# Performance work log

Measured on AMD Instinct MI355X. Metric: run time of the kernel, lower is better.

Reference implementation:

```python
import jax, jax.numpy as jnp
import numpy as np

D_MODEL = 1024
NUM_HEADS = 16
D_K = D_MODEL // NUM_HEADS
B, S = 4, 2048


def setup_inputs() -> dict:
    key = jax.random.key(0)
    ks = jax.random.split(key, 11)
    scale = 1.0 / np.sqrt(D_MODEL)
    inp = {
        "query": jax.random.normal(ks[0], (B, S, D_MODEL), dtype=jnp.float32),
        "key": jax.random.normal(ks[1], (B, S, D_MODEL), dtype=jnp.float32),
        "value": jax.random.normal(ks[2], (B, S, D_MODEL), dtype=jnp.float32),
        "mask": jnp.tril(jnp.ones((S, S), dtype=jnp.int32))[None, None, :, :],
        "Wq": jax.random.normal(ks[3], (D_MODEL, D_MODEL), dtype=jnp.float32) * scale,
        "bq": jax.random.normal(ks[4], (D_MODEL,), dtype=jnp.float32) * scale,
        "Wk": jax.random.normal(ks[5], (D_MODEL, D_MODEL), dtype=jnp.float32) * scale,
        "bk": jax.random.normal(ks[6], (D_MODEL,), dtype=jnp.float32) * scale,
        "Wv": jax.random.normal(ks[7], (D_MODEL, D_MODEL), dtype=jnp.float32) * scale,
        "bv": jax.random.normal(ks[8], (D_MODEL,), dtype=jnp.float32) * scale,
        "Wo": jax.random.normal(ks[9], (D_MODEL, D_MODEL), dtype=jnp.float32) * scale,
        "bo": jax.random.normal(ks[10], (D_MODEL,), dtype=jnp.float32) * scale,
    }
    return inp


def reference(query, key, value, mask, Wq, bq, Wk, bk, Wv, bv, Wo, bo):
    b, s, _ = query.shape
    # Linear projections (torch Linear: x @ W.T + b), split into heads -> [B,H,S,Dk]
    Q = (query @ Wq.T + bq).reshape(b, s, NUM_HEADS, D_K).transpose(0, 2, 1, 3)
    K = (key @ Wk.T + bk).reshape(b, s, NUM_HEADS, D_K).transpose(0, 2, 1, 3)
    V = (value @ Wv.T + bv).reshape(b, s, NUM_HEADS, D_K).transpose(0, 2, 1, 3)
    scores = jnp.einsum("bhqd,bhkd->bhqk", Q, K) / jnp.sqrt(jnp.float32(D_K))
    scores = jnp.where(mask == 0, -jnp.inf, scores)
    attn = jax.nn.softmax(scores, axis=-1)  # dropout p=0.0 -> identity
    x = jnp.einsum("bhqk,bhkd->bhqd", attn, V)
    x = x.transpose(0, 2, 1, 3).reshape(b, s, D_MODEL)
    return x @ Wo.T + bo
```

## Files before the change

### kernel.cpp

```cpp
#include <hip/hip_runtime.h>
#include <cstdint>

#define DM   1024
#define NH   16
#define DKd  64
#define Bb   4
#define Ss   2048

using bf16x8_t = __attribute__((ext_vector_type(8))) __bf16;
using bf16x2_t = __attribute__((ext_vector_type(2))) __bf16;
using f32x4_t  = __attribute__((ext_vector_type(4))) float;
using u16x4_t  = __attribute__((ext_vector_type(4))) unsigned short;
using u16x8_t  = __attribute__((ext_vector_type(8))) unsigned short;
using u32x2_t  = __attribute__((ext_vector_type(2))) unsigned int;

#define MFMA16(a, b, c) __builtin_amdgcn_mfma_f32_16x16x32_bf16((a), (b), (c), 0, 0, 0)

__device__ __forceinline__ void mfma_k16(f32x4_t& c, u32x2_t a, u32x2_t b) {
  asm("v_mfma_f32_16x16x16_bf16 %0, %1, %2, %0" : "+v"(c) : "v"(a), "v"(b));
}

__device__ __forceinline__ unsigned short f2bf(float f) {
  union { float f; unsigned u; } v; v.f = f;
  unsigned r = v.u + 0x7fffu + ((v.u >> 16) & 1u);
  return (unsigned short)(r >> 16);
}

__device__ __forceinline__ void gl16(const void* g, void* l) {
  __builtin_amdgcn_global_load_lds(
      (const __attribute__((address_space(1))) void*)g,
      (__attribute__((address_space(3))) void*)l, 16, 0, 0);
}

struct CvtArgs {
  const float* src[4];
  unsigned short* dst[4];
  int n[4];
};

__global__ void cvt_kernel(CvtArgs a) {
  const int seg = blockIdx.y;
  const float* __restrict__ s = a.src[seg];
  unsigned short* __restrict__ d = a.dst[seg];
  const int n = a.n[seg];
  const int step = gridDim.x * blockDim.x * 4;
  for (int i = (blockIdx.x * blockDim.x + threadIdx.x) * 4; i < n; i += step) {
    f32x4_t v = *(const f32x4_t*)(s + i);
    u16x4_t r;
    r[0] = f2bf(v[0]); r[1] = f2bf(v[1]); r[2] = f2bf(v[2]); r[3] = f2bf(v[3]);
    *(u16x4_t*)(d + i) = r;
  }
}

struct GemmArgs {
  const unsigned short* A[3];
  const float* A32[3];
  const unsigned short* W[3];
  const float* bias[3];
  void* out[3];
  float scl[3];
  int epi[3];
};

__device__ __forceinline__ void gemm_epilogue(
    const GemmArgs& ga, int z, int epi, float scl, const float* bias,
    f32x4_t (&acc)[4][4], int m0, int n0, int wm, int wn, int qr, int kg) {
#pragma unroll
  for (int ni = 0; ni < 4; ++ni) {
    const int col = n0 + wn * 64 + ni * 16 + qr;
    const float bi = bias[col];
#pragma unroll
    for (int mi = 0; mi < 4; ++mi) {
      const int mb = m0 + wm * 64 + mi * 16 + kg * 4;
      float vv[4];
#pragma unroll
      for (int j = 0; j < 4; ++j) vv[j] = (acc[mi][ni][j] + bi) * scl;
      if (epi == 0) {
        unsigned short* O = (unsigned short*)ga.out[z];
#pragma unroll
        for (int j = 0; j < 4; ++j) {
          const int m = mb + j;
          O[(size_t)((m >> 11) * NH + (col >> 6)) * (Ss * DKd) +
            (size_t)(m & (Ss - 1)) * DKd + (col & 63)] = f2bf(vv[j]);
        }
      } else if (epi == 2) {
        unsigned short* O = (unsigned short*)ga.out[z];
        u16x4_t r;
#pragma unroll
        for (int j = 0; j < 4; ++j) r[j] = f2bf(vv[j]);
        const int b = mb >> 11, s = mb & (Ss - 1);
        *(u16x4_t*)&O[((size_t)(b * NH + (col >> 6)) * DKd + (col & 63)) * Ss + s] = r;
      } else {
        float* O = (float*)ga.out[z];
#pragma unroll
        for (int j = 0; j < 4; ++j) O[(size_t)(mb + j) * 1024 + col] = vv[j];
      }
    }
  }
}

__global__ __launch_bounds__(256, 3) void gemm_qkv(GemmArgs ga) {
  const int L = blockIdx.x + 8 * (blockIdx.y + 64 * blockIdx.z);
  const int xcd = L & 7;
  const int sidx = L >> 3;
  const int xw = sidx & 7;
  const int grp = sidx >> 3;
  const int z = grp >> 3;
  const int yw = (grp & 7) * 8 + xcd;

  const float* __restrict__ A32 = ga.A32[z];
  const unsigned short* __restrict__ W = ga.W[z];
  const float* __restrict__ bias = ga.bias[z];
  const float scl = ga.scl[z];
  const int epi = ga.epi[z];

  __shared__ __align__(16) unsigned short sA[128 * 32];
  __shared__ __align__(16) unsigned short sB[2][128 * 32];

  const int tid  = threadIdx.x;
  const int lane = tid & 63;
  const int wid  = tid >> 6;
  const int wm   = wid >> 1, wn = wid & 1;
  const int m0 = yw * 128, n0 = xw * 128;
  const int qr = lane & 15, kg = lane >> 4;

  const int e0 = tid * 8;
  const int e1 = e0 + 2048;
  const int r0 = e0 >> 5, c0 = e0 & 31;
  const int r1 = e1 >> 5, c1 = e1 & 31;

  f32x4_t acc[4][4];
#pragma unroll
  for (int mi = 0; mi < 4; ++mi)
#pragma unroll
    for (int ni = 0; ni < 4; ++ni) acc[mi][ni] = {0.f, 0.f, 0.f, 0.f};

  const float* Ar0 = A32 + (size_t)(m0 + r0) * 1024 + c0;
  const float* Ar1 = A32 + (size_t)(m0 + r1) * 1024 + c1;

  f32x4_t areg[2][4];

#define LDA(par, kn)                                        \
  do {                                                      \
    areg[par][0] = *(const f32x4_t*)(Ar0 + (kn) * 32 + 0);  \
    areg[par][1] = *(const f32x4_t*)(Ar0 + (kn) * 32 + 4);  \
    areg[par][2] = *(const f32x4_t*)(Ar1 + (kn) * 32 + 0);  \
    areg[par][3] = *(const f32x4_t*)(Ar1 + (kn) * 32 + 4);  \
  } while (0)

#define WRA(par)                                            \
  do {                                                      \
    u16x8_t w0_, w1_;                                       \
    _Pragma("unroll") for (int j = 0; j < 4; ++j) {         \
      w0_[j] = f2bf(areg[par][0][j]);                       \
      w0_[4 + j] = f2bf(areg[par][1][j]);                   \
      w1_[j] = f2bf(areg[par][2][j]);                       \
      w1_[4 + j] = f2bf(areg[par][3][j]);                   \
    }                                                       \
    *(u16x8_t*)&sA[e0] = w0_;                               \
    *(u16x8_t*)&sA[e1] = w1_;                               \
  } while (0)

#define LDW(buf, kn)                                                      \
  do {                                                                    \
    gl16(W + (size_t)(n0 + r0) * 1024 + (kn) * 32 + c0, &sB[buf][e0]);    \
    gl16(W + (size_t)(n0 + r1) * 1024 + (kn) * 32 + c1, &sB[buf][e1]);    \
  } while (0)

  LDA(0, 0);
  LDW(0, 0);
  asm volatile("s_waitcnt vmcnt(2)" ::: "memory");
  WRA(0);
  LDA(1, 1);
  LDW(1, 1);
  asm volatile("s_waitcnt vmcnt(6)" ::: "memory");
  asm volatile("s_waitcnt lgkmcnt(0)" ::: "memory");
  __builtin_amdgcn_s_barrier();

#pragma unroll
  for (int kt = 0; kt < 32; ++kt) {
    bf16x8_t af[4], bfr[4];
#pragma unroll
    for (int i = 0; i < 4; ++i) {
      af[i]  = *(const bf16x8_t*)&sA[(wm * 64 + i * 16 + qr) * 32 + kg * 8];
      bfr[i] = *(const bf16x8_t*)&sB[kt & 1][(wn * 64 + i * 16 + qr) * 32 + kg * 8];
    }
    __builtin_amdgcn_s_setprio(1);
#pragma unroll
    for (int mi = 0; mi < 4; ++mi)
#pragma unroll
      for (int ni = 0; ni < 4; ++ni)
        acc[mi][ni] = MFMA16(af[mi], bfr[ni], acc[mi][ni]);
    __builtin_amdgcn_s_setprio(0);
    __builtin_amdgcn_s_barrier();

    if (kt < 31) {
      asm volatile("s_waitcnt vmcnt(2)" ::: "memory");
      WRA((kt + 1) & 1);
      if (kt + 2 < 32) {
        LDA(kt & 1, kt + 2);
        LDW(kt & 1, kt + 2);
        asm volatile("s_waitcnt vmcnt(6)" ::: "memory");
      } else {
        asm volatile("s_waitcnt vmcnt(0)" ::: "memory");
      }
      asm volatile("s_waitcnt lgkmcnt(0)" ::: "memory");
      __builtin_amdgcn_s_barrier();
    }
  }
#undef LDA
#undef WRA
#undef LDW

  gemm_epilogue(ga, z, epi, scl, bias, acc, m0, n0, wm, wn, qr, kg);
}

__global__ __launch_bounds__(256, 4) void gemm_bt(GemmArgs ga) {
  const int L = blockIdx.x + 8 * (blockIdx.y + 64 * blockIdx.z);
  const int xcd = L & 7;
  const int sidx = L >> 3;
  const int xw = sidx & 7;
  const int grp = sidx >> 3;
  const int z = grp >> 3;
  const int yw = (grp & 7) * 8 + xcd;

  const unsigned short* __restrict__ A = ga.A[z];
  const unsigned short* __restrict__ W = ga.W[z];
  const float* __restrict__ bias = ga.bias[z];
  const float scl = ga.scl[z];
  const int epi = ga.epi[z];

  __shared__ __align__(16) unsigned short sA[128 * 32];
  __shared__ __align__(16) unsigned short sB[128 * 32];

  const int tid  = threadIdx.x;
  const int lane = tid & 63;
  const int wid  = tid >> 6;
  const int wm   = wid >> 1, wn = wid & 1;
  const int m0 = yw * 128, n0 = xw * 128;
  const int qr = lane & 15, kg = lane >> 4;

  const int e0 = tid * 8;
  const int e1 = e0 + 2048;
  const int r0 = e0 >> 5, c0 = e0 & 31;
  const int r1 = e1 >> 5, c1 = e1 & 31;

  f32x4_t acc[4][4];
#pragma unroll
  for (int mi = 0; mi < 4; ++mi)
#pragma unroll
    for (int ni = 0; ni < 4; ++ni) acc[mi][ni] = {0.f, 0.f, 0.f, 0.f};

  for (int kt = 0; kt < 32; ++kt) {
    const int k0 = kt * 32;
    gl16(A + (size_t)(m0 + r0) * 1024 + k0 + c0, &sA[e0]);
    gl16(A + (size_t)(m0 + r1) * 1024 + k0 + c1, &sA[e1]);
    gl16(W + (size_t)(n0 + r0) * 1024 + k0 + c0, &sB[e0]);
    gl16(W + (size_t)(n0 + r1) * 1024 + k0 + c1, &sB[e1]);
    __syncthreads();

    bf16x8_t af[4], bfr[4];
#pragma unroll
    for (int i = 0; i < 4; ++i) {
      af[i]  = *(const bf16x8_t*)&sA[(wm * 64 + i * 16 + qr) * 32 + kg * 8];
      bfr[i] = *(const bf16x8_t*)&sB[(wn * 64 + i * 16 + qr) * 32 + kg * 8];
    }
#pragma unroll
    for (int mi = 0; mi < 4; ++mi)
#pragma unroll
      for (int ni = 0; ni < 4; ++ni)
        acc[mi][ni] = MFMA16(af[mi], bfr[ni], acc[mi][ni]);
    __syncthreads();
  }

  gemm_epilogue(ga, z, epi, scl, bias, acc, m0, n0, wm, wn, qr, kg);
}

__global__ __launch_bounds__(256, 3) void attn_kernel(
    const unsigned short* __restrict__ Qp, const unsigned short* __restrict__ Kp,
    const unsigned short* __restrict__ Vt, unsigned short* __restrict__ X) {
  const int x = blockIdx.x, y = blockIdx.y;
  const int bh = x * 8 + (y & 7);
  const int pr = y >> 3;

  const int tid = threadIdx.x, lane = tid & 63, w = tid >> 6;
  const int qr = lane & 15, kg = lane >> 4;

  const unsigned short* Qb = Qp + (size_t)bh * Ss * DKd;
  const unsigned short* Kb = Kp + (size_t)bh * Ss * DKd;
  const unsigned short* Vb = Vt + (size_t)bh * Ss * DKd;

  __shared__ __align__(16) unsigned short kbuf[2][4096];
  __shared__ __align__(16) unsigned short vbuf[2][4096];

  const int R0 = tid >> 3, c80 = (tid & 7) ^ (R0 & 7);
  const int R1 = R0 + 32,  c81 = (tid & 7) ^ (R1 & 7);

  const int bq = bh >> 4, hh = bh & 15;

#pragma unroll
  for (int half = 0; half < 2; ++half) {
    const int jsub = half == 0 ? (15 - pr) : pr;
    const int qbase = jsub * 128;
    const int ntile = 2 * jsub + 2;
    const int qrowA = qbase + w * 32 + qr;
    const int qrowB = qrowA + 16;

    const bf16x8_t qfA0 = *(const bf16x8_t*)&Qb[(size_t)qrowA * DKd + kg * 8];
    const bf16x8_t qfA1 = *(const bf16x8_t*)&Qb[(size_t)qrowA * DKd + 32 + kg * 8];
    const bf16x8_t qfB0 = *(const bf16x8_t*)&Qb[(size_t)qrowB * DKd + kg * 8];
    const bf16x8_t qfB1 = *(const bf16x8_t*)&Qb[(size_t)qrowB * DKd + 32 + kg * 8];

    float lA = 0.f, lB = 0.f;
    f32x4_t o[2][4];
#pragma unroll
    for (int g = 0; g < 2; ++g)
#pragma unroll
      for (int nd = 0; nd < 4; ++nd) o[g][nd] = {0.f, 0.f, 0.f, 0.f};

    int cur = 0;
    gl16(Kb + (size_t)R0 * DKd + c80 * 8, &kbuf[0][tid * 8]);
    gl16(Kb + (size_t)R1 * DKd + c81 * 8, &kbuf[0][tid * 8 + 2048]);
    gl16(Vb + (size_t)R0 * Ss + c80 * 8, &vbuf[0][tid * 8]);
    gl16(Vb + (size_t)R1 * Ss + c81 * 8, &vbuf[0][tid * 8 + 2048]);
    __syncthreads();

    for (int t = 0; t < ntile; ++t) {
      if (t + 1 < ntile) {
        const int kv0 = (t + 1) * 64;
        const int nb = cur ^ 1;
        gl16(Kb + (size_t)(kv0 + R0) * DKd + c80 * 8, &kbuf[nb][tid * 8]);
        gl16(Kb + (size_t)(kv0 + R1) * DKd + c81 * 8, &kbuf[nb][tid * 8 + 2048]);
        gl16(Vb + (size_t)R0 * Ss + kv0 + c80 * 8, &vbuf[nb][tid * 8]);
        gl16(Vb + (size_t)R1 * Ss + kv0 + c81 * 8, &vbuf[nb][tid * 8 + 2048]);
      }

      const bool act = !(w < 2 && t == 2 * jsub + 1);
      if (act) {
        f32x4_t sA_[4], sB_[4];
#pragma unroll
        for (int ni = 0; ni < 4; ++ni) {
          sA_[ni] = {-8.f, -8.f, -8.f, -8.f};
          sB_[ni] = {-8.f, -8.f, -8.f, -8.f};
        }
        __builtin_amdgcn_s_setprio(1);
#pragma unroll
        for (int ni = 0; ni < 4; ++ni) {
          const int R = ni * 16 + qr;
          const bf16x8_t kf0 =
              *(const bf16x8_t*)&kbuf[cur][(R * 8 + (kg ^ (qr & 7))) * 8];
          const bf16x8_t kf1 =
              *(const bf16x8_t*)&kbuf[cur][(R * 8 + ((4 + kg) ^ (qr & 7))) * 8];
          sA_[ni] = MFMA16(kf0, qfA0, sA_[ni]);
          sA_[ni] = MFMA16(kf1, qfA1, sA_[ni]);
          sB_[ni] = MFMA16(kf0, qfB0, sB_[ni]);
          sB_[ni] = MFMA16(kf1, qfB1, sB_[ni]);
        }
        __builtin_amdgcn_s_setprio(0);

        if (t >= 2 * jsub) {
          const int off = (t == 2 * jsub) ? 0 : 64;
          const int rA = w * 32 + qr - off;
#pragma unroll
          for (int ni = 0; ni < 4; ++ni)
#pragma unroll
            for (int j = 0; j < 4; ++j) {
              const int c = ni * 16 + kg * 4 + j;
              if (c > rA) sA_[ni][j] = -1.0e30f;
              if (c > rA + 16) sB_[ni][j] = -1.0e30f;
            }
        }

        u32x2_t pbA[4], pbB[4];
#pragma unroll
        for (int ni = 0; ni < 4; ++ni) {
          float pa0 = exp2f(sA_[ni][0]), pa1 = exp2f(sA_[ni][1]);
          float pa2 = exp2f(sA_[ni][2]), pa3 = exp2f(sA_[ni][3]);
          lA += (pa0 + pa1) + (pa2 + pa3);
          bf16x2_t lo, hi;
          lo[0] = (__bf16)pa0; lo[1] = (__bf16)pa1;
          hi[0] = (__bf16)pa2; hi[1] = (__bf16)pa3;
          pbA[ni][0] = __builtin_bit_cast(unsigned, lo);
          pbA[ni][1] = __builtin_bit_cast(unsigned, hi);
          float pb0 = exp2f(sB_[ni][0]), pb1 = exp2f(sB_[ni][1]);
          float pb2 = exp2f(sB_[ni][2]), pb3 = exp2f(sB_[ni][3]);
          lB += (pb0 + pb1) + (pb2 + pb3);
          bf16x2_t lo2, hi2;
          lo2[0] = (__bf16)pb0; lo2[1] = (__bf16)pb1;
          hi2[0] = (__bf16)pb2; hi2[1] = (__bf16)pb3;
          pbB[ni][0] = __builtin_bit_cast(unsigned, lo2);
          pbB[ni][1] = __builtin_bit_cast(unsigned, hi2);
        }
        asm volatile("s_nop 1");

        __builtin_amdgcn_s_setprio(1);
#pragma unroll
        for (int nd = 0; nd < 4; ++nd) {
          const int rb = (qr + 16 * nd) * 64 + 4 * (kg & 1);
          const int ch = kg >> 1, sw = qr & 7;
          u32x2_t va0 = *(const u32x2_t*)&vbuf[cur][rb + 8 * ((ch + 0) ^ sw)];
          u32x2_t va1 = *(const u32x2_t*)&vbuf[cur][rb + 8 * ((ch + 2) ^ sw)];
          u32x2_t va2 = *(const u32x2_t*)&vbuf[cur][rb + 8 * ((ch + 4) ^ sw)];
          u32x2_t va3 = *(const u32x2_t*)&vbuf[cur][rb + 8 * ((ch + 6) ^ sw)];
          mfma_k16(o[0][nd], va0, pbA[0]);
          mfma_k16(o[0][nd], va1, pbA[1]);
          mfma_k16(o[0][nd], va2, pbA[2]);
          mfma_k16(o[0][nd], va3, pbA[3]);
          mfma_k16(o[1][nd], va0, pbB[0]);
          mfma_k16(o[1][nd], va1, pbB[1]);
          mfma_k16(o[1][nd], va2, pbB[2]);
          mfma_k16(o[1][nd], va3, pbB[3]);
        }
        __builtin_amdgcn_s_setprio(0);
      }

      __syncthreads();
      cur ^= 1;
    }

    float lsA = lA, lsB = lB;
    lsA += __shfl_xor(lsA, 16); lsA += __shfl_xor(lsA, 32);
    lsB += __shfl_xor(lsB, 16); lsB += __shfl_xor(lsB, 32);
    const float invA = 1.0f / lsA, invB = 1.0f / lsB;
#pragma unroll
    for (int nd = 0; nd < 4; ++nd) {
      u16x4_t rA, rB;
#pragma unroll
      for (int j = 0; j < 4; ++j) {
        rA[j] = f2bf(o[0][nd][j] * invA);
        rB[j] = f2bf(o[1][nd][j] * invB);
      }
      const int d = nd * 16 + kg * 4;
      *(u16x4_t*)&X[(size_t)(bq * Ss + qrowA) * DM + hh * DKd + d] = rA;
      *(u16x4_t*)&X[(size_t)(bq * Ss + qrowB) * DM + hh * DKd + d] = rB;
    }
  }
}

extern "C" void kernel_launch(void* const* d_in, const int* in_sizes, int n_in,
                              void* d_out, int out_size, void* d_ws, size_t ws_size,
                              hipStream_t stream) {
  const float* q  = (const float*)d_in[0];
  const float* k  = (const float*)d_in[1];
  const float* v  = (const float*)d_in[2];
  const float* Wq = (const float*)d_in[4];
  const float* bq = (const float*)d_in[5];
  const float* Wk = (const float*)d_in[6];
  const float* bk = (const float*)d_in[7];
  const float* Wv = (const float*)d_in[8];
  const float* bv = (const float*)d_in[9];
  const float* Wo = (const float*)d_in[10];
  const float* bo = (const float*)d_in[11];

  const size_t NIN = (size_t)Bb * Ss * DM;
  const size_t NW  = (size_t)DM * DM;

  unsigned short* ws  = (unsigned short*)d_ws;
  unsigned short* Wqb = ws;
  unsigned short* Wkb = Wqb + NW;
  unsigned short* Wvb = Wkb + NW;
  unsigned short* Wob = Wvb + NW;
  unsigned short* qb  = Wob + NW;
  unsigned short* Qp  = qb + NIN;
  unsigned short* Kp  = Qp + NIN;
  unsigned short* Vt  = Kp + NIN;
  unsigned short* X   = qb;

  CvtArgs ca{};
  ca.src[0] = Wq; ca.dst[0] = Wqb; ca.n[0] = (int)NW;
  ca.src[1] = Wk; ca.dst[1] = Wkb; ca.n[1] = (int)NW;
  ca.src[2] = Wv; ca.dst[2] = Wvb; ca.n[2] = (int)NW;
  ca.src[3] = Wo; ca.dst[3] = Wob; ca.n[3] = (int)NW;
  cvt_kernel<<<dim3(256, 4), 256, 0, stream>>>(ca);

  const float SC = 0.18033688011112042f;

  GemmArgs g1{};
  g1.A32[0] = q;   g1.A32[1] = k;   g1.A32[2] = v;
  g1.W[0] = Wqb;   g1.W[1] = Wkb;   g1.W[2] = Wvb;
  g1.bias[0] = bq; g1.bias[1] = bk; g1.bias[2] = bv;
  g1.out[0] = Qp;  g1.out[1] = Kp;  g1.out[2] = Vt;
  g1.scl[0] = SC;  g1.scl[1] = 1.f; g1.scl[2] = 1.f;
  g1.epi[0] = 0;   g1.epi[1] = 0;   g1.epi[2] = 2;
  gemm_qkv<<<dim3(8, 64, 3), 256, 0, stream>>>(g1);

  attn_kernel<<<dim3(8, 64), 256, 0, stream>>>(Qp, Kp, Vt, X);

  GemmArgs g2{};
  g2.A[0] = X; g2.W[0] = Wob; g2.bias[0] = bo; g2.out[0] = d_out;
  g2.scl[0] = 1.f; g2.epi[0] = 1;
  gemm_bt<<<dim3(8, 64, 1), 256, 0, stream>>>(g2);
}
```

Measured before the change: 179.2 us.

## Load fp32 A tiles directly to LDS and convert to bf16 at fragment read

The QKV projection GEMM now streams fp32 activation tiles straight into shared memory with direct global-to-LDS loads in an XOR-swizzled layout. It converts them to bf16 per fragment when reading, instead of staging through registers and writing bf16 into LDS. The double-buffered, register-prefetched software pipeline is replaced by a single-buffer load/sync/compute/sync loop, and occupancy is raised to 4 blocks. This frees registers and the conversion stores, but loses the overlap of loads with MFMA. It also repeats the fp32-to-bf16 conversion across the two waves that share each A row.

```diff
diff --git a/kernel.cpp b/kernel.cpp
--- a/kernel.cpp
+++ b/kernel.cpp
@@ -99,7 +99,7 @@
   }
 }
 
-__global__ __launch_bounds__(256, 3) void gemm_qkv(GemmArgs ga) {
+__global__ __launch_bounds__(256, 4) void gemm_qkv(GemmArgs ga) {
   const int L = blockIdx.x + 8 * (blockIdx.y + 64 * blockIdx.z);
   const int xcd = L & 7;
   const int sidx = L >> 3;
@@ -114,8 +114,8 @@
   const float scl = ga.scl[z];
   const int epi = ga.epi[z];
 
-  __shared__ __align__(16) unsigned short sA[128 * 32];
-  __shared__ __align__(16) unsigned short sB[2][128 * 32];
+  __shared__ __align__(16) float sA32[128 * 32];
+  __shared__ __align__(16) unsigned short sB[128 * 32];
 
   const int tid  = threadIdx.x;
   const int lane = tid & 63;
@@ -129,61 +129,42 @@
   const int r0 = e0 >> 5, c0 = e0 & 31;
   const int r1 = e1 >> 5, c1 = e1 & 31;
 
+  const int arow = tid >> 3;
+  const int swzc = (tid & 7) ^ ((tid >> 3) & 7);
+
   f32x4_t acc[4][4];
 #pragma unroll
   for (int mi = 0; mi < 4; ++mi)
 #pragma unroll
     for (int ni = 0; ni < 4; ++ni) acc[mi][ni] = {0.f, 0.f, 0.f, 0.f};
 
-  const float* Ar0 = A32 + (size_t)(m0 + r0) * 1024 + c0;
-  const float* Ar1 = A32 + (size_t)(m0 + r1) * 1024 + c1;
-
-  f32x4_t areg[2][4];
-
-#define LDA(par, kn)                                        \
-  do {                                                      \
-    areg[par][0] = *(const f32x4_t*)(Ar0 + (kn) * 32 + 0);  \
-    areg[par][1] = *(const f32x4_t*)(Ar0 + (kn) * 32 + 4);  \
-    areg[par][2] = *(const f32x4_t*)(Ar1 + (kn) * 32 + 0);  \
-    areg[par][3] = *(const f32x4_t*)(Ar1 + (kn) * 32 + 4);  \
-  } while (0)
-
-#define WRA(par)                                            \
-  do {                                                      \
-    u16x8_t w0_, w1_;                                       \
-    _Pragma("unroll") for (int j = 0; j < 4; ++j) {         \
-      w0_[j] = f2bf(areg[par][0][j]);                       \
-      w0_[4 + j] = f2bf(areg[par][1][j]);                   \
-      w1_[j] = f2bf(areg[par][2][j]);                       \
-      w1_[4 + j] = f2bf(areg[par][3][j]);                   \
-    }                                                       \
-    *(u16x8_t*)&sA[e0] = w0_;                               \
-    *(u16x8_t*)&sA[e1] = w1_;                               \
-  } while (0)
-
-#define LDW(buf, kn)                                                      \
-  do {                                                                    \
-    gl16(W + (size_t)(n0 + r0) * 1024 + (kn) * 32 + c0, &sB[buf][e0]);    \
-    gl16(W + (size_t)(n0 + r1) * 1024 + (kn) * 32 + c1, &sB[buf][e1]);    \
-  } while (0)
-
-  LDA(0, 0);
-  LDW(0, 0);
-  asm volatile("s_waitcnt vmcnt(2)" ::: "memory");
-  WRA(0);
-  LDA(1, 1);
-  LDW(1, 1);
-  asm volatile("s_waitcnt vmcnt(6)" ::: "memory");
-  asm volatile("s_waitcnt lgkmcnt(0)" ::: "memory");
-  __builtin_amdgcn_s_barrier();
-
-#pragma unroll
   for (int kt = 0; kt < 32; ++kt) {
+    const int k0 = kt * 32;
+#pragma unroll
+    for (int j = 0; j < 4; ++j)
+      gl16(A32 + (size_t)(m0 + arow + j * 32) * 1024 + k0 + swzc * 4,
+           &sA32[tid * 4 + j * 1024]);
+    gl16(W + (size_t)(n0 + r0) * 1024 + k0 + c0, &sB[e0]);
+    gl16(W + (size_t)(n0 + r1) * 1024 + k0 + c1, &sB[e1]);
+    __syncthreads();
+
     bf16x8_t af[4], bfr[4];
+    const int sw = qr & 7;
 #pragma unroll
     for (int i = 0; i < 4; ++i) {
-      af[i]  = *(const bf16x8_t*)&sA[(wm * 64 + i * 16 + qr) * 32 + kg * 8];
-      bfr[i] = *(const bf16x8_t*)&sB[kt & 1][(wn * 64 + i * 16 + qr) * 32 + kg * 8];
+      const int row = wm * 64 + i * 16 + qr;
+      const f32x4_t alo =
+          *(const f32x4_t*)&sA32[row * 32 + (((2 * kg) ^ sw) << 2)];
+      const f32x4_t ahi =
+          *(const f32x4_t*)&sA32[row * 32 + (((2 * kg + 1) ^ sw) << 2)];
+      u16x8_t aw;
+#pragma unroll
+      for (int j = 0; j < 4; ++j) {
+        aw[j] = f2bf(alo[j]);
+        aw[4 + j] = f2bf(ahi[j]);
+      }
+      af[i] = __builtin_bit_cast(bf16x8_t, aw);
+      bfr[i] = *(const bf16x8_t*)&sB[(wn * 64 + i * 16 + qr) * 32 + kg * 8];
     }
     __builtin_amdgcn_s_setprio(1);
 #pragma unroll
@@ -192,25 +173,8 @@
       for (int ni = 0; ni < 4; ++ni)
         acc[mi][ni] = MFMA16(af[mi], bfr[ni], acc[mi][ni]);
     __builtin_amdgcn_s_setprio(0);
-    __builtin_amdgcn_s_barrier();
-
-    if (kt < 31) {
-      asm volatile("s_waitcnt vmcnt(2)" ::: "memory");
-      WRA((kt + 1) & 1);
-      if (kt + 2 < 32) {
-        LDA(kt & 1, kt + 2);
-        LDW(kt & 1, kt + 2);
-        asm volatile("s_waitcnt vmcnt(6)" ::: "memory");
-      } else {
-        asm volatile("s_waitcnt vmcnt(0)" ::: "memory");
-      }
-      asm volatile("s_waitcnt lgkmcnt(0)" ::: "memory");
-      __builtin_amdgcn_s_barrier();
-    }
+    __syncthreads();
   }
-#undef LDA
-#undef WRA
-#undef LDW
 
   gemm_epilogue(ga, z, epi, scl, bias, acc, m0, n0, wm, wn, qr, kg);
 }
```

Result: slower. 191.5 us (+6.9%).
